# Performance work log

Hardware: AMD Instinct MI355X
Metric: run time of the kernel (lower is better)

Reference implementation:

```python
import jax, jax.numpy as jnp
import numpy as np

N_NODES = 100000
N_EDGES = 1600000
D_IN = 128
D_HID = 128
D_OUT = 64
DROP_P = 0.5


def setup_inputs() -> dict:
    key = jax.random.key(0)
    ks = jax.random.split(key, 8)
    x = jax.random.normal(ks[0], (N_NODES, D_IN), dtype=jnp.float32)
    edge_index = jax.random.randint(ks[1], (2, N_EDGES), 0, N_NODES, dtype=jnp.int64)
    s = lambda fi, fo: 1.0 / np.sqrt(fi)
    W1_l = jax.random.uniform(ks[2], (D_IN, D_HID), jnp.float32, -s(D_IN, D_HID), s(D_IN, D_HID))
    W1_r = jax.random.uniform(ks[3], (D_IN, D_HID), jnp.float32, -s(D_IN, D_HID), s(D_IN, D_HID))
    b1 = jnp.zeros((D_HID,), jnp.float32)
    W2_l = jax.random.uniform(ks[4], (D_HID, D_OUT), jnp.float32, -s(D_HID, D_OUT), s(D_HID, D_OUT))
    W2_r = jax.random.uniform(ks[5], (D_HID, D_OUT), jnp.float32, -s(D_HID, D_OUT), s(D_HID, D_OUT))
    b2 = jnp.zeros((D_OUT,), jnp.float32)
    return {"x": x, "edge_index": edge_index, "W1_l": W1_l, "b1": b1, "W1_r": W1_r,
            "W2_l": W2_l, "b2": b2, "W2_r": W2_r}


def reference(x, edge_index, W1_l, b1, W1_r, W2_l, b2, W2_r):
    N = x.shape[0]
    src = edge_index[0]  # message source x_j
    dst = edge_index[1]  # aggregation target x_i
    # in-degree for mean aggregation (clamped to avoid div-by-zero)
    deg = jax.ops.segment_sum(jnp.ones((src.shape[0],), x.dtype), dst, num_segments=N)
    inv_deg = (1.0 / jnp.maximum(deg, 1.0))[:, None]  # [N,1]

    def sage(h, Wl, b, Wr):
        # mean over incoming neighbors, then lin_l(agg) + bias + lin_r(root)
        agg = jax.ops.segment_sum(h[src], dst, num_segments=N) * inv_deg  # [N,F]
        return agg @ Wl + b + h @ Wr

    h = jax.nn.relu(sage(x, W1_l, b1, W1_r))
    # dropout p=0.5 (training mode), deterministic key
    keep = jax.random.bernoulli(jax.random.key(42), 1.0 - DROP_P, h.shape)
    h = jnp.where(keep, h / (1.0 - DROP_P), 0.0)
    out = sage(h, W2_l, b2, W2_r)
    return jax.nn.log_softmax(out, axis=-1)
```

## Files before the change

kernel.cpp:

```cpp
#include <hip/hip_runtime.h>
#include <stdint.h>

#define D_FEAT 128
#define D_OUT  64
#define BSH 7
#define MAXB 1024
#define BCAP 4096
#define H1P  136
#define SCAT_BLKS 512

typedef __attribute__((ext_vector_type(8))) short short8;
typedef __attribute__((ext_vector_type(8))) ushort ushort8;
typedef __attribute__((ext_vector_type(4))) float f32x4;
typedef __attribute__((ext_vector_type(2))) float f32x2;

__device__ __forceinline__ ushort f2bf(float f) {
  uint32_t u = __float_as_uint(f);
  return (ushort)((u + 0x7FFFu + ((u >> 16) & 1u)) >> 16);
}
__device__ __forceinline__ float bf2f(ushort v) {
  return __uint_as_float((uint32_t)v << 16);
}
__device__ __forceinline__ void acc2(f32x2& a, uint32_t w) {
  f32x2 t;
  t.x = __uint_as_float(w << 16);
  t.y = __uint_as_float(w);
  a += t;
}
__device__ __forceinline__ void accq(f32x2& a, f32x2& b, uint32_t w) {
  a += __builtin_amdgcn_cvt_pk_f32_fp8(w, false);
  b += __builtin_amdgcn_cvt_pk_f32_fp8(w, true);
}

__device__ __forceinline__ void threefry2x32(uint32_t k0, uint32_t k1,
                                             uint32_t& x0, uint32_t& x1) {
  uint32_t k2 = k0 ^ k1 ^ 0x1BD11BDAu;
#define TF_ROT(r) { x0 += x1; x1 = (x1 << (r)) | (x1 >> (32 - (r))); x1 ^= x0; }
  x0 += k0; x1 += k1;
  TF_ROT(13) TF_ROT(15) TF_ROT(26) TF_ROT(6)
  x0 += k1; x1 += k2 + 1u;
  TF_ROT(17) TF_ROT(29) TF_ROT(16) TF_ROT(24)
  x0 += k2; x1 += k0 + 2u;
  TF_ROT(13) TF_ROT(15) TF_ROT(26) TF_ROT(6)
  x0 += k0; x1 += k1 + 3u;
  TF_ROT(17) TF_ROT(29) TF_ROT(16) TF_ROT(24)
  x0 += k1; x1 += k2 + 4u;
  TF_ROT(13) TF_ROT(15) TF_ROT(26) TF_ROT(6)
  x0 += k2; x1 += k0 + 5u;
#undef TF_ROT
}

__device__ __forceinline__ bool keep_bit(uint32_t i) {
  uint32_t t0 = 0u, t1 = i;
  threefry2x32(0u, 42u, t0, t1);
  return (((t0 ^ t1) >> 31) == 0u);
}

__device__ __forceinline__ int load_dst(const void* ei, int is64, long E, long e) {
  return is64 ? (int)((const long long*)ei)[E + e] : ((const int*)ei)[E + e];
}
__device__ __forceinline__ int load_src(const void* ei, int is64, long E, long e) {
  return is64 ? (int)((const long long*)ei)[e] : ((const int*)ei)[e];
}

__global__ __launch_bounds__(256) void prep_kernel(
    const float4* __restrict__ x, const void* __restrict__ ei,
    ushort* __restrict__ xb, uint8_t* __restrict__ xq,
    const float* __restrict__ W1l, const float* __restrict__ W1r,
    const float* __restrict__ W2l, const float* __restrict__ W2r,
    ushort* __restrict__ w1t, ushort* __restrict__ w2lt, ushort* __restrict__ w2rt,
    int* __restrict__ bucketOff, uint32_t* __restrict__ packed,
    long E, long n4, int N, int nbuck, int chunkE, int nConv) {
  const int b = blockIdx.x;
  const int tid = threadIdx.x;

  if (b < SCAT_BLKS) {
    __shared__ int cnt[MAXB];
    __shared__ int base[MAXB];
    __shared__ int cur[MAXB];
    __shared__ int is64_s;
    if (tid < 64) {
      uint32_t v = ((const uint32_t*)ei)[2 * tid + 1];
      unsigned long long nz = __ballot(v != 0u);
      if (tid == 0) is64_s = (nz == 0ull) ? 1 : 0;
    }
    for (int i = tid; i < nbuck; i += 256) { cnt[i] = 0; cur[i] = 0; }
    __syncthreads();
    const int is64 = is64_s;
    long beg = (long)b * chunkE;
    long end = beg + chunkE; if (end > E) end = E;
    for (long e = beg + tid; e < end; e += 256)
      atomicAdd(&cnt[load_dst(ei, is64, E, e) >> BSH], 1);
    __syncthreads();
    for (int i = tid; i < nbuck; i += 256)
      base[i] = cnt[i] ? atomicAdd(&bucketOff[i], cnt[i]) : 0;
    __syncthreads();
    for (long e = beg + tid; e < end; e += 256) {
      int dst = load_dst(ei, is64, E, e);
      int src = load_src(ei, is64, E, e);
      int bk = dst >> BSH;
      int off = atomicAdd(&cur[bk], 1);
      packed[(long)bk * BCAP + base[bk] + off] =
          ((uint32_t)src << BSH) | (uint32_t)(dst & ((1 << BSH) - 1));
    }
  } else if (b < SCAT_BLKS + nConv) {
    long i = (long)(b - SCAT_BLKS) * 256 + tid;
    if (i < n4) {
      float4 v = x[i];
      ushort4 o = {f2bf(v.x), f2bf(v.y), f2bf(v.z), f2bf(v.w)};
      *(ushort4*)(xb + i * 4) = o;
      int p = 0;
      p = __builtin_amdgcn_cvt_pk_fp8_f32(v.x, v.y, p, false);
      p = __builtin_amdgcn_cvt_pk_fp8_f32(v.z, v.w, p, true);
      ((uint32_t*)xq)[i] = (uint32_t)p;
    }
  } else if (b < SCAT_BLKS + nConv + 128) {
    int idx = (b - SCAT_BLKS - nConv) * 256 + tid;
    int j = idx >> 8, k = idx & 255;
    float v = (k < 128) ? W1l[k * 128 + j] : W1r[(k - 128) * 128 + j];
    w1t[j * 256 + k] = f2bf(v);
  } else if (b < SCAT_BLKS + nConv + 128 + 32) {
    int idx = (b - SCAT_BLKS - nConv - 128) * 256 + tid;
    int j = idx >> 7, k = idx & 127;
    w2lt[j * 128 + k] = f2bf(W2l[k * 64 + j]);
  } else if (b < SCAT_BLKS + nConv + 128 + 64) {
    int idx = (b - SCAT_BLKS - nConv - 160) * 256 + tid;
    int j = idx >> 7, k = idx & 127;
    w2rt[j * 128 + k] = f2bf(W2r[k * 64 + j]);
  } else {
    if (tid < 16)
      *(ushort8*)(xb + (long)N * D_FEAT + tid * 8) = (ushort8){0,0,0,0,0,0,0,0};
    else if (tid < 24)
      *(uint4*)(xq + (long)N * D_FEAT + (tid - 16) * 16) = (uint4){0,0,0,0};
  }
}

__global__ __launch_bounds__(256) void bucket_build(
    uint32_t* __restrict__ packed, const int* __restrict__ bucketOff,
    int* __restrict__ rowptr, int* __restrict__ rowend,
    float* __restrict__ invd, int N) {
  __shared__ uint32_t sp[BCAP];
  __shared__ int lcnt[1 << BSH];
  __shared__ int lbase[1 << BSH];
  __shared__ int lcur[1 << BSH];
  const int b = blockIdx.x;
  const int tid = threadIdx.x;
  const int beg = b * BCAP;
  const int cnt = bucketOff[b];
  for (int i = tid; i < cnt; i += 256) sp[i] = packed[beg + i];
  if (tid < 128) { lcnt[tid] = 0; lcur[tid] = 0; }
  __syncthreads();
  for (int i = tid; i < cnt; i += 256)
    atomicAdd(&lcnt[sp[i] & 127], 1);
  __syncthreads();
  if (tid < 128) lbase[tid] = lcnt[tid];
  __syncthreads();
  for (int off = 1; off < 128; off <<= 1) {
    int t = (tid >= off && tid < 128) ? lbase[tid - off] : 0;
    __syncthreads();
    if (tid < 128) lbase[tid] += t;
    __syncthreads();
  }
  if (tid < 128) {
    int excl = lbase[tid] - lcnt[tid];
    lbase[tid] = excl;
    int n = (b << BSH) + tid;
    if (n < N) {
      rowptr[n] = beg + excl;
      rowend[n] = beg + excl + lcnt[tid];
      int d = lcnt[tid];
      invd[n] = 1.0f / (float)(d > 1 ? d : 1);
    }
  }
  __syncthreads();
  for (int i = tid; i < cnt; i += 256) {
    uint32_t p = sp[i];
    int l = p & 127;
    int pos = beg + lbase[l] + atomicAdd(&lcur[l], 1);
    packed[pos] = p >> BSH;
  }
}

__global__ __launch_bounds__(256) void agg_kernel(
    const uint8_t* __restrict__ xq, const int* __restrict__ rowptr,
    const int* __restrict__ rowend, const int* __restrict__ col,
    const float* __restrict__ invd, ushort* __restrict__ aggb,
    unsigned long long* __restrict__ maskb, int N) {
  const int lane = threadIdx.x & 63;
  const int q  = lane >> 4;
  const int sl = lane & 15;
  const uint32_t slb = (uint32_t)sl * 8u;
  int n = (int)(((long)blockIdx.x * blockDim.x + threadIdx.x) >> 6);
  if (n >= N) return;

  {
    uint32_t base = (uint32_t)n * 128u;
    bool k0 = keep_bit(base + (uint32_t)lane);
    bool k1 = keep_bit(base + 64u + (uint32_t)lane);
    unsigned long long w0 = __ballot(k0);
    unsigned long long w1 = __ballot(k1);
    if (lane == 0) {
      maskb[2 * n]     = w0;
      maskb[2 * n + 1] = w1;
    }
  }

  const char* xc = (const char*)xq;
  const int beg = rowptr[n], end = rowend[n];
  const uint32_t zoff = ((uint32_t)N << 7) + slb;

  f32x2 acc[4];
#pragma unroll
  for (int i = 0; i < 4; i++) acc[i] = (f32x2){0.f, 0.f};

  for (int e = beg + q; e < end; e += 16) {
    int c0 = col[e], c1 = col[e + 4], c2 = col[e + 8], c3 = col[e + 12];
    uint32_t o0 = ((uint32_t)c0 << 7) + slb;
    uint32_t o1 = (e + 4  < end) ? (((uint32_t)c1 << 7) + slb) : zoff;
    uint32_t o2 = (e + 8  < end) ? (((uint32_t)c2 << 7) + slb) : zoff;
    uint32_t o3 = (e + 12 < end) ? (((uint32_t)c3 << 7) + slb) : zoff;
    uint2 a = *(const uint2*)(xc + o0);
    uint2 b = *(const uint2*)(xc + o1);
    uint2 c = *(const uint2*)(xc + o2);
    uint2 d = *(const uint2*)(xc + o3);
    accq(acc[0], acc[1], a.x); accq(acc[2], acc[3], a.y);
    accq(acc[0], acc[1], b.x); accq(acc[2], acc[3], b.y);
    accq(acc[0], acc[1], c.x); accq(acc[2], acc[3], c.y);
    accq(acc[0], acc[1], d.x); accq(acc[2], acc[3], d.y);
  }

#pragma unroll
  for (int i = 0; i < 4; i++) {
    acc[i].x += __shfl_xor(acc[i].x, 16);
    acc[i].y += __shfl_xor(acc[i].y, 16);
    acc[i].x += __shfl_xor(acc[i].x, 32);
    acc[i].y += __shfl_xor(acc[i].y, 32);
  }

  if (q == 0) {
    float sc = invd[n];
    ushort8 o;
#pragma unroll
    for (int i = 0; i < 4; i++) {
      o[2 * i]     = f2bf(acc[i].x * sc);
      o[2 * i + 1] = f2bf(acc[i].y * sc);
    }
    *(ushort8*)(aggb + (long)n * D_FEAT + sl * 8) = o;
  }
}

__global__ __launch_bounds__(256) void fused12_kernel(
    const ushort* __restrict__ aggb, const ushort* __restrict__ xb,
    const ushort* __restrict__ w1t, const float* __restrict__ b1,
    const unsigned long long* __restrict__ maskb,
    const ushort* __restrict__ w2lt, const ushort* __restrict__ w2rt,
    const float* __restrict__ b2,
    uint8_t* __restrict__ y2q, ushort* __restrict__ z, int N) {
  __shared__ __align__(16) ushort smem[33792];
  ushort* w1s = smem;
  ushort* h1s = smem;
  ushort* wsl = smem + 17408;
  ushort* wsr = smem + 25600;

  const int tid = threadIdx.x;
  const int lane = tid & 63;
  const int wv = tid >> 6;
  const int r16 = lane & 15;
  const int kg = lane >> 4;

  if (blockIdx.x == 0 && tid < 4)
    ((uint4*)(y2q + (long)N * D_OUT))[tid] = (uint4){0, 0, 0, 0};

  {
    const uint32_t swz = ((uint32_t)(tid >> 5) & 7u) << 4;
#pragma unroll
    for (int i = 0; i < 16; i++) {
      uint32_t byte = (uint32_t)i * 4096u + (uint32_t)tid * 16u;
      uint4 v = *(const uint4*)((const char*)w1t + byte);
      *(uint4*)((char*)w1s + (byte ^ swz)) = v;
    }
  }
  __syncthreads();

  const int node_base = blockIdx.x * 128 + wv * 32;
  int ar0 = node_base + r16;       if (ar0 >= N) ar0 = N - 1;
  int ar1 = node_base + 16 + r16;  if (ar1 >= N) ar1 = N - 1;

  f32x4 acc0[8], acc1[8];
#pragma unroll
  for (int i = 0; i < 8; i++) {
    acc0[i] = (f32x4){0.f, 0.f, 0.f, 0.f};
    acc1[i] = (f32x4){0.f, 0.f, 0.f, 0.f};
  }

  {
    const ushort* a0g = aggb + (long)ar0 * 128 + kg * 8;
    const ushort* a0x = xb   + (long)ar0 * 128 + kg * 8;
    const ushort* a1g = aggb + (long)ar1 * 128 + kg * 8;
    const ushort* a1x = xb   + (long)ar1 * 128 + kg * 8;
    const uint32_t rswz = ((uint32_t)(r16 & 7)) << 4;
#pragma unroll
    for (int s = 0; s < 8; s++) {
      short8 aT0 = (s < 4) ? *(const short8*)(a0g + s * 32)
                           : *(const short8*)(a0x + (s - 4) * 32);
      short8 aT1 = (s < 4) ? *(const short8*)(a1g + s * 32)
                           : *(const short8*)(a1x + (s - 4) * 32);
#pragma unroll
      for (int ct = 0; ct < 8; ct++) {
        uint32_t boff = ((uint32_t)(ct * 16 + r16) * 512u +
                         (uint32_t)s * 64u + (uint32_t)kg * 16u) ^ rswz;
        short8 b = *(const short8*)((const char*)w1s + boff);
        acc0[ct] = __builtin_amdgcn_mfma_f32_16x16x32_bf16(aT0, b, acc0[ct], 0, 0, 0);
        acc1[ct] = __builtin_amdgcn_mfma_f32_16x16x32_bf16(aT1, b, acc1[ct], 0, 0, 0);
      }
    }
  }
  __syncthreads();

  {
    const uint32_t swz = ((uint32_t)(tid >> 4) & 7u) << 4;
#pragma unroll
    for (int i = 0; i < 4; i++) {
      uint32_t byte = (uint32_t)i * 4096u + (uint32_t)tid * 16u;
      uint4 vl = *(const uint4*)((const char*)w2lt + byte);
      uint4 vr = *(const uint4*)((const char*)w2rt + byte);
      *(uint4*)((char*)wsl + (byte ^ swz)) = vl;
      *(uint4*)((char*)wsr + (byte ^ swz)) = vr;
    }
  }

  {
    float bbv[8];
#pragma unroll
    for (int ct = 0; ct < 8; ct++) bbv[ct] = b1[ct * 16 + r16];
#pragma unroll
    for (int t = 0; t < 2; t++) {
      const f32x4* acc = t ? acc1 : acc0;
#pragma unroll
      for (int r = 0; r < 4; r++) {
        int row_l = wv * 32 + t * 16 + kg * 4 + r;
        int n = blockIdx.x * 128 + row_l;
        int mi = (n < N) ? n : (N - 1);
        unsigned long long m0 = maskb[2 * mi];
        unsigned long long m1 = maskb[2 * mi + 1];
        ushort* dst = h1s + row_l * H1P + r16;
#pragma unroll
        for (int ct = 0; ct < 8; ct++) {
          int j = ct * 16 + r16;
          float h = fmaxf(acc[ct][r] + bbv[ct], 0.f);
          unsigned long long w = (j & 64) ? m1 : m0;
          bool keep = (w >> (j & 63)) & 1ull;
          dst[ct * 16] = keep ? f2bf(2.0f * h) : (ushort)0;
        }
      }
    }
  }
  __syncthreads();

  f32x4 aL[2][4], aR[2][4];
#pragma unroll
  for (int t = 0; t < 2; t++)
#pragma unroll
    for (int i = 0; i < 4; i++) {
      aL[t][i] = (f32x4){0.f, 0.f, 0.f, 0.f};
      aR[t][i] = (f32x4){0.f, 0.f, 0.f, 0.f};
    }

  {
    const uint32_t rswz = ((uint32_t)(r16 & 7)) << 4;
#pragma unroll
    for (int s = 0; s < 4; s++) {
#pragma unroll
      for (int t = 0; t < 2; t++) {
        const ushort* ap = h1s + (wv * 32 + t * 16 + r16) * H1P + s * 32 + kg * 8;
        short8 a = *(const short8*)ap;
#pragma unroll
        for (int ct = 0; ct < 4; ct++) {
          uint32_t boff = ((uint32_t)(ct * 16 + r16) * 256u +
                           (uint32_t)s * 64u + (uint32_t)kg * 16u) ^ rswz;
          short8 bl = *(const short8*)((const char*)wsl + boff);
          short8 br = *(const short8*)((const char*)wsr + boff);
          aL[t][ct] = __builtin_amdgcn_mfma_f32_16x16x32_bf16(a, bl, aL[t][ct], 0, 0, 0);
          aR[t][ct] = __builtin_amdgcn_mfma_f32_16x16x32_bf16(a, br, aR[t][ct], 0, 0, 0);
        }
      }
    }
  }

  float bb[4];
#pragma unroll
  for (int ct = 0; ct < 4; ct++) bb[ct] = b2[ct * 16 + r16];

#pragma unroll
  for (int t = 0; t < 2; t++) {
    int nb = node_base + t * 16;
#pragma unroll
    for (int r = 0; r < 4; r++) {
      int n = nb + kg * 4 + r;
      if (n < N) {
#pragma unroll
        for (int ct = 0; ct < 4; ct++) {
          float yv = aL[t][ct][r];
          int p = __builtin_amdgcn_cvt_pk_fp8_f32(yv, yv, 0, false);
          y2q[(long)n * D_OUT + ct * 16 + r16] = (uint8_t)p;
          z  [(long)n * D_OUT + ct * 16 + r16] = f2bf(aR[t][ct][r] + bb[ct]);
        }
      }
    }
  }
}

__global__ __launch_bounds__(256) void agg64_kernel(
    const uint8_t* __restrict__ y2q, const ushort* __restrict__ z,
    const int* __restrict__ rowptr, const int* __restrict__ rowend,
    const int* __restrict__ col, const float* __restrict__ invd,
    float* __restrict__ out, int N) {
  const int lane = threadIdx.x & 63;
  const int g  = lane >> 3;
  const int sl = lane & 7;
  const uint32_t slb = (uint32_t)sl * 8u;
  int n = (int)(((long)blockIdx.x * blockDim.x + threadIdx.x) >> 6);
  if (n >= N) return;

  const char* xc = (const char*)y2q;
  const int beg = rowptr[n], end = rowend[n];
  const uint32_t zoff = ((uint32_t)N << 6) + slb;

  f32x2 acc[4];
#pragma unroll
  for (int i = 0; i < 4; i++) acc[i] = (f32x2){0.f, 0.f};

  for (int e = beg + g; e < end; e += 16) {
    int c0 = col[e], c1 = col[e + 8];
    uint32_t o0 = ((uint32_t)c0 << 6) + slb;
    uint32_t o1 = (e + 8 < end) ? (((uint32_t)c1 << 6) + slb) : zoff;
    uint2 a = *(const uint2*)(xc + o0);
    uint2 b = *(const uint2*)(xc + o1);
    accq(acc[0], acc[1], a.x); accq(acc[2], acc[3], a.y);
    accq(acc[0], acc[1], b.x); accq(acc[2], acc[3], b.y);
  }

#pragma unroll
  for (int i = 0; i < 4; i++) {
    acc[i].x += __shfl_xor(acc[i].x, 8);
    acc[i].y += __shfl_xor(acc[i].y, 8);
    acc[i].x += __shfl_xor(acc[i].x, 16);
    acc[i].y += __shfl_xor(acc[i].y, 16);
    acc[i].x += __shfl_xor(acc[i].x, 32);
    acc[i].y += __shfl_xor(acc[i].y, 32);
  }

  if (g == 0) {
    float sc = invd[n];
    ushort8 zr = *(const ushort8*)(z + (long)n * D_OUT + sl * 8);
    float v[8];
#pragma unroll
    for (int i = 0; i < 4; i++) {
      v[2 * i]     = acc[i].x * sc + bf2f(zr[2 * i]);
      v[2 * i + 1] = acc[i].y * sc + bf2f(zr[2 * i + 1]);
    }
    float m = v[0];
#pragma unroll
    for (int j = 1; j < 8; j++) m = fmaxf(m, v[j]);
    m = fmaxf(m, __shfl_xor(m, 1));
    m = fmaxf(m, __shfl_xor(m, 2));
    m = fmaxf(m, __shfl_xor(m, 4));
    float s = 0.f;
#pragma unroll
    for (int j = 0; j < 8; j++) s += expf(v[j] - m);
    s += __shfl_xor(s, 1);
    s += __shfl_xor(s, 2);
    s += __shfl_xor(s, 4);
    float ls = m + logf(s);
    float4 o0 = {v[0] - ls, v[1] - ls, v[2] - ls, v[3] - ls};
    float4 o1 = {v[4] - ls, v[5] - ls, v[6] - ls, v[7] - ls};
    float* op = out + (long)n * D_OUT + sl * 8;
    *(float4*)op = o0;
    *(float4*)(op + 4) = o1;
  }
}

extern "C" void kernel_launch(void* const* d_in, const int* in_sizes, int n_in,
                              void* d_out, int out_size, void* d_ws, size_t ws_size,
                              hipStream_t stream) {
  const float* x   = (const float*)d_in[0];
  const void*  ei  = d_in[1];
  const float* W1l = (const float*)d_in[2];
  const float* b1  = (const float*)d_in[3];
  const float* W1r = (const float*)d_in[4];
  const float* W2l = (const float*)d_in[5];
  const float* b2  = (const float*)d_in[6];
  const float* W2r = (const float*)d_in[7];
  float* out = (float*)d_out;

  const int  N  = in_sizes[0] / D_FEAT;
  const long E  = (long)in_sizes[1] / 2;
  const long NF = (long)N * D_FEAT;
  const int  nbuck = (N + (1 << BSH) - 1) >> BSH;

  char* ws = (char*)d_ws;
  size_t off = 0;
  auto alloc = [&](size_t bytes) -> void* {
    void* p = ws + off;
    off = (off + bytes + 255) & ~(size_t)255;
    return p;
  };
  int*      bucketOff = (int*)alloc(sizeof(int) * MAXB);
  int*      rowptr    = (int*)alloc(sizeof(int) * N);
  int*      rowend    = (int*)alloc(sizeof(int) * N);
  uint32_t* packed    = (uint32_t*)alloc(sizeof(uint32_t) * ((size_t)nbuck * BCAP + 16));
  float*    invd      = (float*)alloc(sizeof(float) * N);
  ushort*   xb        = (ushort*)alloc(sizeof(ushort) * (NF + D_FEAT));
  uint8_t*  xq        = (uint8_t*)alloc(sizeof(uint8_t) * (NF + D_FEAT));
  ushort*   aggb      = (ushort*)alloc(sizeof(ushort) * NF);
  ushort*   z         = (ushort*)alloc(sizeof(ushort) * ((size_t)N * D_OUT + 256));
  ushort*   w1t       = (ushort*)alloc(sizeof(ushort) * 128 * 256);
  ushort*   w2lt      = (ushort*)alloc(sizeof(ushort) * 64 * 128);
  ushort*   w2rt      = (ushort*)alloc(sizeof(ushort) * 64 * 128);
  unsigned long long* maskb = (unsigned long long*)alloc(sizeof(unsigned long long) * 2 * N);

  int* col = (int*)packed;
  uint8_t* y2q = xq;

  const long n4 = NF / 4;
  const int nConv = (int)((n4 + 255) / 256);
  const int chunkE = (int)((E + SCAT_BLKS - 1) / SCAT_BLKS);
  const int prepBlocks = SCAT_BLKS + nConv + 128 + 64 + 1;

  hipMemsetAsync(bucketOff, 0, sizeof(int) * MAXB, stream);

  prep_kernel<<<prepBlocks, 256, 0, stream>>>(
      (const float4*)x, ei, xb, xq, W1l, W1r, W2l, W2r,
      w1t, w2lt, w2rt, bucketOff, packed,
      E, n4, N, nbuck, chunkE, nConv);

  bucket_build<<<nbuck, 256, 0, stream>>>(packed, bucketOff, rowptr, rowend, invd, N);

  const int aggBlocks = (int)(((long)N * 64 + 255) / 256);
  const int gemmBlocks = (N + 127) / 128;

  agg_kernel<<<aggBlocks, 256, 0, stream>>>(xq, rowptr, rowend, col, invd, aggb, maskb, N);
  fused12_kernel<<<gemmBlocks, 256, 0, stream>>>(aggb, xb, w1t, b1, maskb,
                                                 w2lt, w2rt, b2, y2q, z, N);
  agg64_kernel<<<aggBlocks, 256, 0, stream>>>(y2q, z, rowptr, rowend, col, invd, out, N);
}
```

Measured before the change: 184.8 us.

## Split weight staging in fused layer kernel to shrink shared memory

Cuts the fused layer-1/layer-2 kernel's shared memory from about 66KB to 50KB. W1 is now staged in two K-halves (aggregate part, then root part), and W2_l and W2_r take turns in a single buffer. The goal is more resident blocks per CU so global loads overlap better. The cost is extra __syncthreads barriers and serialized weight loads, and h1 fragments are now held in registers across both layer-2 GEMMs.

After: 196.2 us. 6.2% more time.

```diff
diff --git a/kernel.cpp b/kernel.cpp
--- a/kernel.cpp
+++ b/kernel.cpp
@@ -256,31 +256,20 @@
     const ushort* __restrict__ w2lt, const ushort* __restrict__ w2rt,
     const float* __restrict__ b2,
     uint8_t* __restrict__ y2q, ushort* __restrict__ z, int N) {
-  __shared__ __align__(16) ushort smem[33792];
+  __shared__ __align__(16) ushort smem[25600];
   ushort* w1s = smem;
   ushort* h1s = smem;
-  ushort* wsl = smem + 17408;
-  ushort* wsr = smem + 25600;
+  ushort* wb  = smem + 17408;
 
   const int tid = threadIdx.x;
   const int lane = tid & 63;
   const int wv = tid >> 6;
   const int r16 = lane & 15;
   const int kg = lane >> 4;
+  const uint32_t rswz = ((uint32_t)(r16 & 7)) << 4;
 
   if (blockIdx.x == 0 && tid < 4)
     ((uint4*)(y2q + (long)N * D_OUT))[tid] = (uint4){0, 0, 0, 0};
-
-  {
-    const uint32_t swz = ((uint32_t)(tid >> 5) & 7u) << 4;
-#pragma unroll
-    for (int i = 0; i < 16; i++) {
-      uint32_t byte = (uint32_t)i * 4096u + (uint32_t)tid * 16u;
-      uint4 v = *(const uint4*)((const char*)w1t + byte);
-      *(uint4*)((char*)w1s + (byte ^ swz)) = v;
-    }
-  }
-  __syncthreads();
 
   const int node_base = blockIdx.x * 128 + wv * 32;
   int ar0 = node_base + r16;       if (ar0 >= N) ar0 = N - 1;
@@ -293,29 +282,36 @@
     acc1[i] = (f32x4){0.f, 0.f, 0.f, 0.f};
   }
 
-  {
-    const ushort* a0g = aggb + (long)ar0 * 128 + kg * 8;
-    const ushort* a0x = xb   + (long)ar0 * 128 + kg * 8;
-    const ushort* a1g = aggb + (long)ar1 * 128 + kg * 8;
-    const ushort* a1x = xb   + (long)ar1 * 128 + kg * 8;
-    const uint32_t rswz = ((uint32_t)(r16 & 7)) << 4;
-#pragma unroll
-    for (int s = 0; s < 8; s++) {
-      short8 aT0 = (s < 4) ? *(const short8*)(a0g + s * 32)
-                           : *(const short8*)(a0x + (s - 4) * 32);
-      short8 aT1 = (s < 4) ? *(const short8*)(a1g + s * 32)
-                           : *(const short8*)(a1x + (s - 4) * 32);
+#pragma unroll
+  for (int h = 0; h < 2; h++) {
+    {
+#pragma unroll
+      for (int i = 0; i < 8; i++) {
+        uint32_t dst = (uint32_t)i * 4096u + (uint32_t)tid * 16u;
+        uint32_t row = dst >> 8;
+        uint4 v = *(const uint4*)((const char*)w1t +
+                                  (row << 9) + (uint32_t)(h << 8) + (dst & 255u));
+        *(uint4*)((char*)w1s + (dst ^ ((row & 7u) << 4))) = v;
+      }
+    }
+    __syncthreads();
+    const ushort* a0p = (h == 0 ? aggb : xb) + (long)ar0 * 128 + kg * 8;
+    const ushort* a1p = (h == 0 ? aggb : xb) + (long)ar1 * 128 + kg * 8;
+#pragma unroll
+    for (int s = 0; s < 4; s++) {
+      short8 aT0 = *(const short8*)(a0p + s * 32);
+      short8 aT1 = *(const short8*)(a1p + s * 32);
 #pragma unroll
       for (int ct = 0; ct < 8; ct++) {
-        uint32_t boff = ((uint32_t)(ct * 16 + r16) * 512u +
+        uint32_t boff = ((uint32_t)(ct * 16 + r16) * 256u +
                          (uint32_t)s * 64u + (uint32_t)kg * 16u) ^ rswz;
         short8 b = *(const short8*)((const char*)w1s + boff);
         acc0[ct] = __builtin_amdgcn_mfma_f32_16x16x32_bf16(aT0, b, acc0[ct], 0, 0, 0);
         acc1[ct] = __builtin_amdgcn_mfma_f32_16x16x32_bf16(aT1, b, acc1[ct], 0, 0, 0);
       }
     }
-  }
-  __syncthreads();
+    __syncthreads();
+  }
 
   {
     const uint32_t swz = ((uint32_t)(tid >> 4) & 7u) << 4;
@@ -323,12 +319,9 @@
     for (int i = 0; i < 4; i++) {
       uint32_t byte = (uint32_t)i * 4096u + (uint32_t)tid * 16u;
       uint4 vl = *(const uint4*)((const char*)w2lt + byte);
-      uint4 vr = *(const uint4*)((const char*)w2rt + byte);
-      *(uint4*)((char*)wsl + (byte ^ swz)) = vl;
-      *(uint4*)((char*)wsr + (byte ^ swz)) = vr;
-    }
-  }
-
+      *(uint4*)((char*)wb + (byte ^ swz)) = vl;
+    }
+  }
   {
     float bbv[8];
 #pragma unroll
@@ -357,35 +350,59 @@
   }
   __syncthreads();
 
-  f32x4 aL[2][4], aR[2][4];
+  short8 af[2][4];
 #pragma unroll
   for (int t = 0; t < 2; t++)
 #pragma unroll
+    for (int s = 0; s < 4; s++)
+      af[t][s] = *(const short8*)(h1s + (wv * 32 + t * 16 + r16) * H1P +
+                                  s * 32 + kg * 8);
+
+  f32x4 aL[2][4];
+#pragma unroll
+  for (int t = 0; t < 2; t++)
+#pragma unroll
+    for (int i = 0; i < 4; i++) aL[t][i] = (f32x4){0.f, 0.f, 0.f, 0.f};
+#pragma unroll
+  for (int s = 0; s < 4; s++)
+#pragma unroll
+    for (int t = 0; t < 2; t++)
+#pragma unroll
+      for (int ct = 0; ct < 4; ct++) {
+        uint32_t boff = ((uint32_t)(ct * 16 + r16) * 256u +
+                         (uint32_t)s * 64u + (uint32_t)kg * 16u) ^ rswz;
+        short8 bl = *(const short8*)((const char*)wb + boff);
+        aL[t][ct] = __builtin_amdgcn_mfma_f32_16x16x32_bf16(af[t][s], bl, aL[t][ct], 0, 0, 0);
+      }
+  __syncthreads();
+
+  {
+    const uint32_t swz = ((uint32_t)(tid >> 4) & 7u) << 4;
+#pragma unroll
     for (int i = 0; i < 4; i++) {
-      aL[t][i] = (f32x4){0.f, 0.f, 0.f, 0.f};
-      aR[t][i] = (f32x4){0.f, 0.f, 0.f, 0.f};
-    }
-
-  {
-    const uint32_t rswz = ((uint32_t)(r16 & 7)) << 4;
-#pragma unroll
-    for (int s = 0; s < 4; s++) {
-#pragma unroll
-      for (int t = 0; t < 2; t++) {
-        const ushort* ap = h1s + (wv * 32 + t * 16 + r16) * H1P + s * 32 + kg * 8;
-        short8 a = *(const short8*)ap;
-#pragma unroll
-        for (int ct = 0; ct < 4; ct++) {
-          uint32_t boff = ((uint32_t)(ct * 16 + r16) * 256u +
-                           (uint32_t)s * 64u + (uint32_t)kg * 16u) ^ rswz;
-          short8 bl = *(const short8*)((const char*)wsl + boff);
-          short8 br = *(const short8*)((const char*)wsr + boff);
-          aL[t][ct] = __builtin_amdgcn_mfma_f32_16x16x32_bf16(a, bl, aL[t][ct], 0, 0, 0);
-          aR[t][ct] = __builtin_amdgcn_mfma_f32_16x16x32_bf16(a, br, aR[t][ct], 0, 0, 0);
-        }
+      uint32_t byte = (uint32_t)i * 4096u + (uint32_t)tid * 16u;
+      uint4 vr = *(const uint4*)((const char*)w2rt + byte);
+      *(uint4*)((char*)wb + (byte ^ swz)) = vr;
+    }
+  }
+  __syncthreads();
+
+  f32x4 aR[2][4];
+#pragma unroll
+  for (int t = 0; t < 2; t++)
+#pragma unroll
+    for (int i = 0; i < 4; i++) aR[t][i] = (f32x4){0.f, 0.f, 0.f, 0.f};
+#pragma unroll
+  for (int s = 0; s < 4; s++)
+#pragma unroll
+    for (int t = 0; t < 2; t++)
+#pragma unroll
+      for (int ct = 0; ct < 4; ct++) {
+        uint32_t boff = ((uint32_t)(ct * 16 + r16) * 256u +
+                         (uint32_t)s * 64u + (uint32_t)kg * 16u) ^ rswz;
+        short8 br = *(const short8*)((const char*)wb + boff);
+        aR[t][ct] = __builtin_amdgcn_mfma_f32_16x16x32_bf16(af[t][s], br, aR[t][ct], 0, 0, 0);
       }
-    }
-  }
 
   float bb[4];
 #pragma unroll
```
